# Optimization experiments

Hardware: AMD Instinct MI355X
Metric: run time of the kernel (lower is better)

## Reference

```python
import jax, jax.numpy as jnp
import numpy as np

PAIRS = np.array([[0, 4], [1, 5], [2, 6], [3, 7], [0, 5], [1, 4], [2, 7], [3, 6]])


def setup_inputs() -> dict:
    key = jax.random.key(0)
    ks = jax.random.split(key, 40)
    rn = lambda k, shape: (jax.random.normal(k, shape, jnp.float32) * 0.05)
    inp = {
        "waiting": jax.random.uniform(ks[0], (1, 8), jnp.float32),
        "phase": jax.random.uniform(ks[1], (1, 8), jnp.float32),
        "wtime_mu": jax.random.uniform(ks[2], (1, 8), jnp.float32),
        "wtime_sigma": jax.random.uniform(ks[3], (1, 8), jnp.float32),
        "wtime_max": jax.random.uniform(ks[4], (1, 8), jnp.float32),
        "i_position": jax.random.uniform(ks[5], (1, 1), jnp.float32),
        "j_position": jax.random.uniform(ks[6], (1, 1), jnp.float32),
        # NN_demand: 14 -> 256 -> 32 -> 4
        "d_w1": rn(ks[7], (256, 14)), "d_b1": rn(ks[8], (256,)),
        "d_w2": rn(ks[9], (32, 256)), "d_b2": rn(ks[10], (32,)),
        "d_w3": rn(ks[11], (4, 32)), "d_b3": rn(ks[12], (4,)),
        # NN_coupled_demand: 8 -> 128 -> 32 -> 4
        "c_w1": rn(ks[13], (128, 8)), "c_b1": rn(ks[14], (128,)),
        "c_w2": rn(ks[15], (32, 128)), "c_b2": rn(ks[16], (32,)),
        "c_w3": rn(ks[17], (4, 32)), "c_b3": rn(ks[18], (4,)),
        # Conv_D: 1x1 convs 8 -> 256 -> 32 -> 2
        "dD_w1": rn(ks[19], (256, 8)), "dD_b1": rn(ks[20], (256,)),
        "dD_w2": rn(ks[21], (32, 256)), "dD_b2": rn(ks[22], (32,)),
        "dD_w3": rn(ks[23], (2, 32)), "dD_b3": rn(ks[24], (2,)),
        # Conv_C: 1x1 convs 3 -> 256 -> 32 -> 8, then (1,7) conv 8 -> 1
        "cC_w1": rn(ks[25], (256, 3)), "cC_b1": rn(ks[26], (256,)),
        "cC_w2": rn(ks[27], (32, 256)), "cC_b2": rn(ks[28], (32,)),
        "cC_w3": rn(ks[29], (8, 32)), "cC_b3": rn(ks[30], (8,)),
        "cC_w4": rn(ks[31], (8, 7)), "cC_b4": rn(ks[32], (1,)),
    }
    return inp


def _mlp3(x, w1, b1, w2, b2, w3, b3):
    h = jax.nn.relu(x @ w1.T + b1)
    h = jax.nn.relu(h @ w2.T + b2)
    return h @ w3.T + b3


def _frap_forward(waiting, phase, wtime_mu, wtime_sigma, wtime_max, i_position, j_position,
                  d_w1, d_b1, d_w2, d_b2, d_w3, d_b3,
                  c_w1, c_b1, c_w2, c_b2, c_w3, c_b3,
                  dD_w1, dD_b1, dD_w2, dD_b2, dD_w3, dD_b3,
                  cC_w1, cC_b1, cC_w2, cC_b2, cC_w3, cC_b3, cC_w4, cC_b4):
    pairs = jnp.asarray(PAIRS)
    # per-lane demand features: (8, 14) = [i, j, mu_l, sigma_l, max_l, wait_l, phase(8)]
    feat = jnp.concatenate([
        jnp.broadcast_to(i_position[0], (8, 1)),
        jnp.broadcast_to(j_position[0], (8, 1)),
        wtime_mu[0, :, None], wtime_sigma[0, :, None],
        wtime_max[0, :, None], waiting[0, :, None],
        jnp.broadcast_to(phase[0][None, :], (8, 8)),
    ], axis=1)
    demand = _mlp3(feat, d_w1, d_b1, d_w2, d_b2, d_w3, d_b3)  # (8, 4)
    # coupled demand per phase pair: (8, 8) -> (8, 4)
    vec = jnp.concatenate([demand[pairs[:, 0]], demand[pairs[:, 1]]], axis=1)
    dp = _mlp3(vec, c_w1, c_b1, c_w2, c_b2, c_w3, c_b3)  # (8, 4)
    # D tensor (8, 8, 7): D[0:4, i, k] = dp[i]; D[4:8, i, k] = dp[j(k)], j(k)=k + (k>=i)
    k = jnp.arange(7)
    i = jnp.arange(8)
    j_idx = k[None, :] + (k[None, :] >= i[:, None]).astype(jnp.int32)  # (8, 7)
    top = jnp.broadcast_to(dp.T[:, :, None], (4, 8, 7))
    bot = jnp.transpose(dp[j_idx], (2, 0, 1))  # (4, 8, 7)
    D = jnp.concatenate([top, bot], axis=0)  # (8, 8, 7)
    # Conv_D: 1x1 convs are channel matmuls on (C, H, W)
    h = jax.nn.relu(jnp.einsum('oc,chw->ohw', dD_w1, D) + dD_b1[:, None, None])
    h = jax.nn.relu(jnp.einsum('oc,chw->ohw', dD_w2, h) + dD_b2[:, None, None])
    H_d = jnp.einsum('oc,chw->ohw', dD_w3, h) + dD_b3[:, None, None]  # (2, 8, 7)
    comp = jnp.zeros((1, 8, 7), H_d.dtype)
    H_c = jnp.concatenate([H_d, comp], axis=0)  # (3, 8, 7)
    # Conv_C
    h = jax.nn.relu(jnp.einsum('oc,chw->ohw', cC_w1, H_c) + cC_b1[:, None, None])
    h = jax.nn.relu(jnp.einsum('oc,chw->ohw', cC_w2, h) + cC_b2[:, None, None])
    h = jax.nn.relu(jnp.einsum('oc,chw->ohw', cC_w3, h) + cC_b3[:, None, None])  # (8, 8, 7)
    # conv4: kernel (1,7), out (1, 8, 1); return C[0, :, 0] -> (8,)
    out = jnp.einsum('cw,chw->h', cC_w4, h) + cC_b4[0]
    return out


def reference(waiting, phase, wtime_mu, wtime_sigma, wtime_max, i_position, j_position,
              d_w1, d_b1, d_w2, d_b2, d_w3, d_b3,
              c_w1, c_b1, c_w2, c_b2, c_w3, c_b3,
              dD_w1, dD_b1, dD_w2, dD_b2, dD_w3, dD_b3,
              cC_w1, cC_b1, cC_w2, cC_b2, cC_w3, cC_b3, cC_w4, cC_b4):
    return _frap_forward(waiting, phase, wtime_mu, wtime_sigma, wtime_max, i_position, j_position,
                         d_w1, d_b1, d_w2, d_b2, d_w3, d_b3,
                         c_w1, c_b1, c_w2, c_b2, c_w3, c_b3,
                         dD_w1, dD_b1, dD_w2, dD_b2, dD_w3, dD_b3,
                         cC_w1, cC_b1, cC_w2, cC_b2, cC_w3, cC_b3, cC_w4, cC_b4)
```

## Files before the change

kernel.cpp:

```cpp
#include <hip/hip_runtime.h>


#define DEV __device__ __forceinline__

#define WAVE_SYNC() do { \
    asm volatile("s_waitcnt lgkmcnt(0)" ::: "memory"); \
    __builtin_amdgcn_sched_barrier(0); \
} while (0)

DEV float dot4a(float acc, float4 a, float4 b) {
    acc = fmaf(a.x, b.x, acc);
    acc = fmaf(a.y, b.y, acc);
    acc = fmaf(a.z, b.z, acc);
    acc = fmaf(a.w, b.w, acc);
    return acc;
}

DEV float warm_arr(const float* __restrict__ p, int n4, int id, float sink) {
    const float4* p4 = (const float4*)p;
    for (int i = id; i < n4; i += 448) {
        float4 v = p4[i];
        sink += v.x + v.y + v.z + v.w;
    }
    return sink;
}

DEV void conv_h2_vec(const float* __restrict__ big, const float* __restrict__ w2g,
                     const float* __restrict__ b2g, float* __restrict__ mid, int t)
{
    int kq = t & 1;
    int u  = t >> 1;
    int ch = u >> 3, sl = u & 7;
    float a0 = 0.0f, a1 = 0.0f, a2 = 0.0f, a3 = 0.0f;
    if (sl < 7) {
        const float4* wp = (const float4*)(w2g + ch * 256) + kq * 32;
        const float* hrow = big + (sl << 8);
#pragma unroll 2
        for (int g = 0; g < 32; g += 4) {
            int gg = kq * 32 + g;
            float4 w0 = wp[g + 0], w1 = wp[g + 1], w2 = wp[g + 2], w3 = wp[g + 3];
            float4 h0 = *(const float4*)(hrow + (((gg + 0) ^ sl) << 2));
            float4 h1 = *(const float4*)(hrow + (((gg + 1) ^ sl) << 2));
            float4 h2 = *(const float4*)(hrow + (((gg + 2) ^ sl) << 2));
            float4 h3v = *(const float4*)(hrow + (((gg + 3) ^ sl) << 2));
            a0 = dot4a(a0, h0, w0);
            a1 = dot4a(a1, h1, w1);
            a2 = dot4a(a2, h2, w2);
            a3 = dot4a(a3, h3v, w3);
        }
    }
    float r = (a0 + a1) + (a2 + a3);
    r += __shfl_xor(r, 1);
    if (sl < 7 && kq == 0)
        mid[ch * 7 + sl] = fmaxf(r + b2g[ch], 0.0f);
}

__global__ __launch_bounds__(512, 1) void frap_kernel(
    const float* __restrict__ waiting, const float* __restrict__ phase,
    const float* __restrict__ wtime_mu, const float* __restrict__ wtime_sigma,
    const float* __restrict__ wtime_max,
    const float* __restrict__ i_pos, const float* __restrict__ j_pos,
    const float* __restrict__ d_w1, const float* __restrict__ d_b1,
    const float* __restrict__ d_w2, const float* __restrict__ d_b2,
    const float* __restrict__ d_w3, const float* __restrict__ d_b3,
    const float* __restrict__ c_w1, const float* __restrict__ c_b1,
    const float* __restrict__ c_w2, const float* __restrict__ c_b2,
    const float* __restrict__ c_w3, const float* __restrict__ c_b3,
    const float* __restrict__ dD_w1, const float* __restrict__ dD_b1,
    const float* __restrict__ dD_w2, const float* __restrict__ dD_b2,
    const float* __restrict__ dD_w3, const float* __restrict__ dD_b3,
    const float* __restrict__ cC_w1, const float* __restrict__ cC_b1,
    const float* __restrict__ cC_w2, const float* __restrict__ cC_b2,
    const float* __restrict__ cC_w3, const float* __restrict__ cC_b3,
    const float* __restrict__ cC_w4, const float* __restrict__ cC_b4,
    float* __restrict__ out)
{
    __shared__ __align__(16) float sm[4096];
    const int t  = threadIdx.x;
    const int wg = blockIdx.x;
    const int ln = t & 63;

    float* feat16 = sm;
    float* dh1  = sm + 128;
    float* dh2  = sm + 2176;
    float* dem  = sm + 2432;
    float* ch1  = sm + 2464;
    float* ch2  = sm + 3488;
    float* big  = sm;
    float* mid  = sm + 3744;
    float* dp   = sm + 3968;
    float* Hd   = sm + 4000;
    float* h3   = sm;

    if (t < 64) {
        for (int rep = 0; rep < 2; ++rep) {
            int idx = rep * 64 + ln;
            int l = idx >> 4, c = idx & 15;
            float v = 0.0f;
            if      (c == 0) v = i_pos[0];
            else if (c == 1) v = j_pos[0];
            else if (c == 2) v = wtime_mu[l];
            else if (c == 3) v = wtime_sigma[l];
            else if (c == 4) v = wtime_max[l];
            else if (c == 5) v = waiting[l];
            else if (c < 14) v = phase[c - 6];
            feat16[idx] = v;
        }
        WAVE_SYNC();

        for (int q = 0; q < 4; ++q) {
            int o = q * 64 + ln;
            const float* w = d_w1 + o * 14;
            float w0 = w[0], w1 = w[1], w2 = w[2], w3 = w[3], w4 = w[4];
            float w5 = w[5], w6 = w[6], w7 = w[7], w8 = w[8], w9 = w[9];
            float wa = w[10], wb = w[11], wc = w[12], wd = w[13];
            float bias = d_b1[o];
#pragma unroll
            for (int l = 0; l < 8; ++l) {
                const float4* f4 = (const float4*)(feat16 + l * 16);
                float4 f0 = f4[0], f1 = f4[1], f2 = f4[2], f3 = f4[3];
                float acc = bias;
                acc = fmaf(f0.x, w0, acc); acc = fmaf(f0.y, w1, acc);
                acc = fmaf(f0.z, w2, acc); acc = fmaf(f0.w, w3, acc);
                acc = fmaf(f1.x, w4, acc); acc = fmaf(f1.y, w5, acc);
                acc = fmaf(f1.z, w6, acc); acc = fmaf(f1.w, w7, acc);
                acc = fmaf(f2.x, w8, acc); acc = fmaf(f2.y, w9, acc);
                acc = fmaf(f2.z, wa, acc); acc = fmaf(f2.w, wb, acc);
                acc = fmaf(f3.x, wc, acc); acc = fmaf(f3.y, wd, acc);
                dh1[l * 256 + o] = fmaxf(acc, 0.0f);
            }
        }
        WAVE_SYNC();

        {
            int o = ln & 31, lh = ln >> 5;
            float acc0 = 0.0f, acc1 = 0.0f, acc2 = 0.0f, acc3 = 0.0f;
            const float4* w4p = (const float4*)(d_w2 + o * 256);
#pragma unroll 4
            for (int cb = 0; cb < 64; ++cb) {
                float4 w = w4p[cb];
                float4 h0 = *(const float4*)(dh1 + (lh * 4 + 0) * 256 + cb * 4);
                float4 h1 = *(const float4*)(dh1 + (lh * 4 + 1) * 256 + cb * 4);
                float4 h2 = *(const float4*)(dh1 + (lh * 4 + 2) * 256 + cb * 4);
                float4 h3v = *(const float4*)(dh1 + (lh * 4 + 3) * 256 + cb * 4);
                acc0 = dot4a(acc0, h0, w);
                acc1 = dot4a(acc1, h1, w);
                acc2 = dot4a(acc2, h2, w);
                acc3 = dot4a(acc3, h3v, w);
            }
            float b = d_b2[o];
            dh2[(lh * 4 + 0) * 32 + o] = fmaxf(acc0 + b, 0.0f);
            dh2[(lh * 4 + 1) * 32 + o] = fmaxf(acc1 + b, 0.0f);
            dh2[(lh * 4 + 2) * 32 + o] = fmaxf(acc2 + b, 0.0f);
            dh2[(lh * 4 + 3) * 32 + o] = fmaxf(acc3 + b, 0.0f);
        }
        WAVE_SYNC();

        if (ln < 32) {
            int l = ln >> 2, o = ln & 3;
            const float4* w = (const float4*)(d_w3 + o * 32);
            const float4* h = (const float4*)(dh2 + l * 32);
            float acc = d_b3[o];
#pragma unroll
            for (int g = 0; g < 8; ++g) acc = dot4a(acc, h[g], w[g]);
            dem[ln] = acc;
        }
        WAVE_SYNC();

        for (int rep = 0; rep < 2; ++rep) {
            int o = rep * 64 + ln;
            const float4* w = (const float4*)(c_w1 + o * 8);
            float4 w0 = w[0], w1 = w[1];
            float bias = c_b1[o];
#pragma unroll
            for (int p = 0; p < 8; ++p) {
                int a0 = p & 3;
                int a1 = (p < 4) ? (4 + (p & 3)) : (4 + ((p & 3) ^ 1));
                float4 va = *(const float4*)(dem + a0 * 4);
                float4 vb = *(const float4*)(dem + a1 * 4);
                float acc = dot4a(dot4a(bias, va, w0), vb, w1);
                ch1[p * 128 + o] = fmaxf(acc, 0.0f);
            }
        }
        WAVE_SYNC();

        {
            int o = ln & 31, lh = ln >> 5;
            float acc0 = 0.0f, acc1 = 0.0f, acc2 = 0.0f, acc3 = 0.0f;
            const float4* w4p = (const float4*)(c_w2 + o * 128);
#pragma unroll 4
            for (int cb = 0; cb < 32; ++cb) {
                float4 w = w4p[cb];
                float4 h0 = *(const float4*)(ch1 + (lh * 4 + 0) * 128 + cb * 4);
                float4 h1 = *(const float4*)(ch1 + (lh * 4 + 1) * 128 + cb * 4);
                float4 h2 = *(const float4*)(ch1 + (lh * 4 + 2) * 128 + cb * 4);
                float4 h3v = *(const float4*)(ch1 + (lh * 4 + 3) * 128 + cb * 4);
                acc0 = dot4a(acc0, h0, w);
                acc1 = dot4a(acc1, h1, w);
                acc2 = dot4a(acc2, h2, w);
                acc3 = dot4a(acc3, h3v, w);
            }
            float b = c_b2[o];
            ch2[(lh * 4 + 0) * 32 + o] = fmaxf(acc0 + b, 0.0f);
            ch2[(lh * 4 + 1) * 32 + o] = fmaxf(acc1 + b, 0.0f);
            ch2[(lh * 4 + 2) * 32 + o] = fmaxf(acc2 + b, 0.0f);
            ch2[(lh * 4 + 3) * 32 + o] = fmaxf(acc3 + b, 0.0f);
        }
        WAVE_SYNC();

        if (ln < 32) {
            int l = ln >> 2, o = ln & 3;
            const float4* w = (const float4*)(c_w3 + o * 32);
            const float4* h = (const float4*)(ch2 + l * 32);
            float acc = c_b3[o];
#pragma unroll
            for (int g = 0; g < 8; ++g) acc = dot4a(acc, h[g], w[g]);
            dp[ln] = acc;
        }
    } else {
        int id = t - 64;
        float snk = 0.0f;
        snk = warm_arr(d_w1,  896, id, snk);
        snk = warm_arr(d_b1,   64, id, snk);
        snk = warm_arr(d_w2, 2048, id, snk);
        snk = warm_arr(d_b2,    8, id, snk);
        snk = warm_arr(d_w3,   32, id, snk);
        snk = warm_arr(d_b3,    1, id, snk);
        snk = warm_arr(c_w1,  256, id, snk);
        snk = warm_arr(c_b1,   32, id, snk);
        snk = warm_arr(c_w2, 1024, id, snk);
        snk = warm_arr(c_b2,    8, id, snk);
        snk = warm_arr(c_w3,   32, id, snk);
        snk = warm_arr(c_b3,    1, id, snk);
        snk = warm_arr(dD_w1, 512, id, snk);
        snk = warm_arr(dD_b1,  64, id, snk);
        snk = warm_arr(dD_w2, 2048, id, snk);
        snk = warm_arr(dD_b2,   8, id, snk);
        snk = warm_arr(dD_w3,  16, id, snk);
        snk = warm_arr(cC_w1, 192, id, snk);
        snk = warm_arr(cC_b1,  64, id, snk);
        snk = warm_arr(cC_w2, 2048, id, snk);
        snk = warm_arr(cC_b2,   8, id, snk);
        snk = warm_arr(cC_w3,  64, id, snk);
        snk = warm_arr(cC_b3,   2, id, snk);
        snk = warm_arr(cC_w4,  14, id, snk);
        asm volatile("" :: "v"(snk));
    }
    __syncthreads();

    {
        const float4* dp4 = (const float4*)dp;
        int o = t & 255;
        const float4* wrow = (const float4*)(dD_w1 + o * 8);
        float4 w0 = wrow[0], w1 = wrow[1];
        float bias = dD_b1[o];
        float4 di = dp4[wg];
#pragma unroll
        for (int it = 0; it < 4; ++it) {
            int sl = (t >> 8) + it * 2;
            if (sl < 7) {
                int j = sl + (sl >= wg ? 1 : 0);
                float acc = dot4a(dot4a(bias, di, w0), dp4[j], w1);
                big[(sl << 8) + (((o >> 2) ^ sl) << 2) + (o & 3)] = fmaxf(acc, 0.0f);
            }
        }
    }
    __syncthreads();

    conv_h2_vec(big, dD_w2, dD_b2, mid, t);
    __syncthreads();

    if (t < 56) {
        int kq = t & 3, u = t >> 2;
        int o = (u >= 7) ? 1 : 0;
        int s = u - o * 7;
        float acc = 0.0f;
#pragma unroll
        for (int cc = 0; cc < 8; ++cc) {
            int c = kq * 8 + cc;
            acc = fmaf(mid[c * 7 + s], dD_w3[o * 32 + c], acc);
        }
        acc += __shfl_xor(acc, 1);
        acc += __shfl_xor(acc, 2);
        if (kq == 0) Hd[o * 7 + s] = acc + dD_b3[o];
    }
    __syncthreads();

    {
        int o = t & 255;
        float w0 = cC_w1[o * 3], w1 = cC_w1[o * 3 + 1];
        float bias = cC_b1[o];
#pragma unroll
        for (int it = 0; it < 4; ++it) {
            int sl = (t >> 8) + it * 2;
            if (sl < 7) {
                float acc = fmaf(Hd[7 + sl], w1, fmaf(Hd[sl], w0, bias));
                big[(sl << 8) + (((o >> 2) ^ sl) << 2) + (o & 3)] = fmaxf(acc, 0.0f);
            }
        }
    }
    __syncthreads();

    conv_h2_vec(big, cC_w2, cC_b2, mid, t);
    __syncthreads();

    if (t < 224) {
        int kq = t & 3, u = t >> 2;
        int o = u & 7, s = u >> 3;
        float acc = 0.0f;
#pragma unroll
        for (int cc = 0; cc < 8; ++cc) {
            int c = kq * 8 + cc;
            acc = fmaf(mid[c * 7 + s], cC_w3[o * 32 + c], acc);
        }
        acc += __shfl_xor(acc, 1);
        acc += __shfl_xor(acc, 2);
        if (kq == 0) h3[o * 7 + s] = fmaxf(acc + cC_b3[o], 0.0f);
    }
    __syncthreads();

    if (t < 64) {
        float p = 0.0f;
        if (ln < 56) {
            int c = ln / 7, w = ln % 7;
            p = cC_w4[c * 7 + w] * h3[c * 7 + w];
        }
#pragma unroll
        for (int off = 1; off < 64; off <<= 1) p += __shfl_xor(p, off);
        if (ln == 0) out[wg] = p + cC_b4[0];
    }
}

extern "C" void kernel_launch(void* const* d_in, const int* in_sizes, int n_in,
                              void* d_out, int out_size, void* d_ws, size_t ws_size,
                              hipStream_t stream) {
    (void)in_sizes; (void)n_in; (void)d_ws; (void)ws_size; (void)out_size;
    const float* a[33];
    for (int i = 0; i < 33; ++i) a[i] = (const float*)d_in[i];
    frap_kernel<<<dim3(8), dim3(512), 0, stream>>>(
        a[0], a[1], a[2], a[3], a[4], a[5], a[6],
        a[7], a[8], a[9], a[10], a[11], a[12],
        a[13], a[14], a[15], a[16], a[17], a[18],
        a[19], a[20], a[21], a[22], a[23], a[24],
        a[25], a[26], a[27], a[28], a[29], a[30], a[31], a[32],
        (float*)d_out);
}
```

Baseline: 26.35 us.

## Assign one wave per spatial column to run the conv chain without block barriers

Restructures the Conv_D/Conv_C stages so each of 7 waves handles one spatial position end to end, chaining the layers with wave-local LDS waits instead of several block-wide __syncthreads. Each wave's partial of the final (1,7) conv goes to shared memory, and a single thread sums the seven partials. This removes about six block barriers and the cross-position shared layout. In exchange, each wave now does serial work (64 lanes per 256-wide layer), leaves one of the eight waves idle, and makes each wave reload the weights itself.

```diff
diff --git a/kernel.cpp b/kernel.cpp
--- a/kernel.cpp
+++ b/kernel.cpp
@@ -23,36 +23,6 @@
         sink += v.x + v.y + v.z + v.w;
     }
     return sink;
-}
-
-DEV void conv_h2_vec(const float* __restrict__ big, const float* __restrict__ w2g,
-                     const float* __restrict__ b2g, float* __restrict__ mid, int t)
-{
-    int kq = t & 1;
-    int u  = t >> 1;
-    int ch = u >> 3, sl = u & 7;
-    float a0 = 0.0f, a1 = 0.0f, a2 = 0.0f, a3 = 0.0f;
-    if (sl < 7) {
-        const float4* wp = (const float4*)(w2g + ch * 256) + kq * 32;
-        const float* hrow = big + (sl << 8);
-#pragma unroll 2
-        for (int g = 0; g < 32; g += 4) {
-            int gg = kq * 32 + g;
-            float4 w0 = wp[g + 0], w1 = wp[g + 1], w2 = wp[g + 2], w3 = wp[g + 3];
-            float4 h0 = *(const float4*)(hrow + (((gg + 0) ^ sl) << 2));
-            float4 h1 = *(const float4*)(hrow + (((gg + 1) ^ sl) << 2));
-            float4 h2 = *(const float4*)(hrow + (((gg + 2) ^ sl) << 2));
-            float4 h3v = *(const float4*)(hrow + (((gg + 3) ^ sl) << 2));
-            a0 = dot4a(a0, h0, w0);
-            a1 = dot4a(a1, h1, w1);
-            a2 = dot4a(a2, h2, w2);
-            a3 = dot4a(a3, h3v, w3);
-        }
-    }
-    float r = (a0 + a1) + (a2 + a3);
-    r += __shfl_xor(r, 1);
-    if (sl < 7 && kq == 0)
-        mid[ch * 7 + sl] = fmaxf(r + b2g[ch], 0.0f);
 }
 
 __global__ __launch_bounds__(512, 1) void frap_kernel(
@@ -86,11 +56,12 @@
     float* dem  = sm + 2432;
     float* ch1  = sm + 2464;
     float* ch2  = sm + 3488;
-    float* big  = sm;
-    float* mid  = sm + 3744;
+    float* conv_h1   = sm;
+    float* conv_mid  = sm + 1792;
+    float* conv_mid2 = sm + 2016;
+    float* conv_Hd   = sm + 2240;
+    float* partial   = sm + 2254;
     float* dp   = sm + 3968;
-    float* Hd   = sm + 4000;
-    float* h3   = sm;
 
     if (t < 64) {
         for (int rep = 0; rep < 2; ++rep) {
@@ -249,85 +220,105 @@
     __syncthreads();
 
     {
-        const float4* dp4 = (const float4*)dp;
-        int o = t & 255;
-        const float4* wrow = (const float4*)(dD_w1 + o * 8);
-        float4 w0 = wrow[0], w1 = wrow[1];
-        float bias = dD_b1[o];
-        float4 di = dp4[wg];
-#pragma unroll
-        for (int it = 0; it < 4; ++it) {
-            int sl = (t >> 8) + it * 2;
-            if (sl < 7) {
-                int j = sl + (sl >= wg ? 1 : 0);
-                float acc = dot4a(dot4a(bias, di, w0), dp4[j], w1);
-                big[(sl << 8) + (((o >> 2) ^ sl) << 2) + (o & 3)] = fmaxf(acc, 0.0f);
+        int w = t >> 6;
+        if (w < 7) {
+            const int j = w + (w >= wg ? 1 : 0);
+            float* h1row = conv_h1  + w * 256;
+            float* midp  = conv_mid + w * 32;
+            float* mid2p = conv_mid2 + w * 32;
+            float* Hdp   = conv_Hd  + w * 2;
+
+            const float4* dp4 = (const float4*)dp;
+            float4 di = dp4[wg], dj = dp4[j];
+#pragma unroll
+            for (int q = 0; q < 4; ++q) {
+                int o = q * 64 + ln;
+                const float4* wrow = (const float4*)(dD_w1 + o * 8);
+                float acc = dot4a(dot4a(dD_b1[o], di, wrow[0]), dj, wrow[1]);
+                h1row[o] = fmaxf(acc, 0.0f);
+            }
+            WAVE_SYNC();
+
+            {
+                int ch = ln >> 1, kq = ln & 1;
+                const float4* wp = (const float4*)(dD_w2 + ch * 256) + kq * 32;
+                const float4* hp = (const float4*)h1row + kq * 32;
+                float a0 = 0.0f, a1 = 0.0f, a2 = 0.0f, a3 = 0.0f;
+#pragma unroll 2
+                for (int e = 0; e < 32; e += 4) {
+                    a0 = dot4a(a0, hp[e + 0], wp[e + 0]);
+                    a1 = dot4a(a1, hp[e + 1], wp[e + 1]);
+                    a2 = dot4a(a2, hp[e + 2], wp[e + 2]);
+                    a3 = dot4a(a3, hp[e + 3], wp[e + 3]);
+                }
+                float r = (a0 + a1) + (a2 + a3);
+                r += __shfl_xor(r, 1);
+                if (kq == 0) midp[ch] = fmaxf(r + dD_b2[ch], 0.0f);
+            }
+            WAVE_SYNC();
+
+            if (ln < 2) {
+                const float4* wp = (const float4*)(dD_w3 + ln * 32);
+                const float4* mp = (const float4*)midp;
+                float acc = dD_b3[ln];
+#pragma unroll
+                for (int g = 0; g < 8; ++g) acc = dot4a(acc, mp[g], wp[g]);
+                Hdp[ln] = acc;
+            }
+            WAVE_SYNC();
+
+            {
+                float h0 = Hdp[0], h1v = Hdp[1];
+#pragma unroll
+                for (int q = 0; q < 4; ++q) {
+                    int o = q * 64 + ln;
+                    float acc = fmaf(h1v, cC_w1[o * 3 + 1],
+                                     fmaf(h0, cC_w1[o * 3], cC_b1[o]));
+                    h1row[o] = fmaxf(acc, 0.0f);
+                }
+            }
+            WAVE_SYNC();
+
+            {
+                int ch = ln >> 1, kq = ln & 1;
+                const float4* wp = (const float4*)(cC_w2 + ch * 256) + kq * 32;
+                const float4* hp = (const float4*)h1row + kq * 32;
+                float a0 = 0.0f, a1 = 0.0f, a2 = 0.0f, a3 = 0.0f;
+#pragma unroll 2
+                for (int e = 0; e < 32; e += 4) {
+                    a0 = dot4a(a0, hp[e + 0], wp[e + 0]);
+                    a1 = dot4a(a1, hp[e + 1], wp[e + 1]);
+                    a2 = dot4a(a2, hp[e + 2], wp[e + 2]);
+                    a3 = dot4a(a3, hp[e + 3], wp[e + 3]);
+                }
+                float r = (a0 + a1) + (a2 + a3);
+                r += __shfl_xor(r, 1);
+                if (kq == 0) mid2p[ch] = fmaxf(r + cC_b2[ch], 0.0f);
+            }
+            WAVE_SYNC();
+
+            if (ln < 8) {
+                const float4* wp = (const float4*)(cC_w3 + ln * 32);
+                const float4* mp = (const float4*)mid2p;
+                float acc = cC_b3[ln];
+#pragma unroll
+                for (int g = 0; g < 8; ++g) acc = dot4a(acc, mp[g], wp[g]);
+                float h3v = fmaxf(acc, 0.0f);
+                float p = cC_w4[ln * 7 + w] * h3v;
+                p += __shfl_xor(p, 1);
+                p += __shfl_xor(p, 2);
+                p += __shfl_xor(p, 4);
+                if (ln == 0) partial[w] = p;
             }
         }
     }
     __syncthreads();
 
-    conv_h2_vec(big, dD_w2, dD_b2, mid, t);
-    __syncthreads();
-
-    if (t < 56) {
-        int kq = t & 3, u = t >> 2;
-        int o = (u >= 7) ? 1 : 0;
-        int s = u - o * 7;
-        float acc = 0.0f;
-#pragma unroll
-        for (int cc = 0; cc < 8; ++cc) {
-            int c = kq * 8 + cc;
-            acc = fmaf(mid[c * 7 + s], dD_w3[o * 32 + c], acc);
-        }
-        acc += __shfl_xor(acc, 1);
-        acc += __shfl_xor(acc, 2);
-        if (kq == 0) Hd[o * 7 + s] = acc + dD_b3[o];
-    }
-    __syncthreads();
-
-    {
-        int o = t & 255;
-        float w0 = cC_w1[o * 3], w1 = cC_w1[o * 3 + 1];
-        float bias = cC_b1[o];
-#pragma unroll
-        for (int it = 0; it < 4; ++it) {
-            int sl = (t >> 8) + it * 2;
-            if (sl < 7) {
-                float acc = fmaf(Hd[7 + sl], w1, fmaf(Hd[sl], w0, bias));
-                big[(sl << 8) + (((o >> 2) ^ sl) << 2) + (o & 3)] = fmaxf(acc, 0.0f);
-            }
-        }
-    }
-    __syncthreads();
-
-    conv_h2_vec(big, cC_w2, cC_b2, mid, t);
-    __syncthreads();
-
-    if (t < 224) {
-        int kq = t & 3, u = t >> 2;
-        int o = u & 7, s = u >> 3;
-        float acc = 0.0f;
-#pragma unroll
-        for (int cc = 0; cc < 8; ++cc) {
-            int c = kq * 8 + cc;
-            acc = fmaf(mid[c * 7 + s], cC_w3[o * 32 + c], acc);
-        }
-        acc += __shfl_xor(acc, 1);
-        acc += __shfl_xor(acc, 2);
-        if (kq == 0) h3[o * 7 + s] = fmaxf(acc + cC_b3[o], 0.0f);
-    }
-    __syncthreads();
-
-    if (t < 64) {
-        float p = 0.0f;
-        if (ln < 56) {
-            int c = ln / 7, w = ln % 7;
-            p = cC_w4[c * 7 + w] * h3[c * 7 + w];
-        }
-#pragma unroll
-        for (int off = 1; off < 64; off <<= 1) p += __shfl_xor(p, off);
-        if (ln == 0) out[wg] = p + cC_b4[0];
+    if (t == 0) {
+        float s = cC_b4[0];
+#pragma unroll
+        for (int w = 0; w < 7; ++w) s += partial[w];
+        out[wg] = s;
     }
 }
 
```

Result: slower. 30.98 us (+17.6%).

## Split demand MLPs across two waves and fuse Conv_D tail into Conv_C input

Applied to the files above, without the earlier changes.

The demand and coupled-demand MLP stages now run on two waves, each handling half the rows, with a block barrier between the two MLPs. Cache warming moves to the remaining waves and is split across those phases. The Conv_D final layer is fused with the Conv_C first layer per wave, which removes one block barrier. The Conv_C final layer is likewise fused with the (1,7) conv through per-wave partial sums, removing another barrier. The trade-off is an extra __syncthreads between the MLPs and redundant per-wave recomputation of Hd.

```diff
diff --git a/kernel.cpp b/kernel.cpp
--- a/kernel.cpp
+++ b/kernel.cpp
@@ -18,7 +18,7 @@
 
 DEV float warm_arr(const float* __restrict__ p, int n4, int id, float sink) {
     const float4* p4 = (const float4*)p;
-    for (int i = id; i < n4; i += 448) {
+    for (int i = id; i < n4; i += 384) {
         float4 v = p4[i];
         sink += v.x + v.y + v.z + v.w;
     }
@@ -78,6 +78,7 @@
     __shared__ __align__(16) float sm[4096];
     const int t  = threadIdx.x;
     const int wg = blockIdx.x;
+    const int wv = t >> 6;
     const int ln = t & 63;
 
     float* feat16 = sm;
@@ -86,15 +87,15 @@
     float* dem  = sm + 2432;
     float* ch1  = sm + 2464;
     float* ch2  = sm + 3488;
-    float* big  = sm;
-    float* mid  = sm + 3744;
     float* dp   = sm + 3968;
-    float* Hd   = sm + 4000;
-    float* h3   = sm;
-
-    if (t < 64) {
-        for (int rep = 0; rep < 2; ++rep) {
-            int idx = rep * 64 + ln;
+    float* convh   = sm;
+    float* mid     = sm + 1792;
+    float* partial = sm + 2016;
+
+    if (wv < 2) {
+        const int wbase = wv * 4;
+        {
+            int idx = wv * 64 + ln;
             int l = idx >> 4, c = idx & 15;
             float v = 0.0f;
             if      (c == 0) v = i_pos[0];
@@ -116,7 +117,8 @@
             float wa = w[10], wb = w[11], wc = w[12], wd = w[13];
             float bias = d_b1[o];
 #pragma unroll
-            for (int l = 0; l < 8; ++l) {
+            for (int r = 0; r < 4; ++r) {
+                int l = wbase + r;
                 const float4* f4 = (const float4*)(feat16 + l * 16);
                 float4 f0 = f4[0], f1 = f4[1], f2 = f4[2], f3 = f4[3];
                 float acc = bias;
@@ -134,91 +136,34 @@
 
         {
             int o = ln & 31, lh = ln >> 5;
-            float acc0 = 0.0f, acc1 = 0.0f, acc2 = 0.0f, acc3 = 0.0f;
+            int r0 = wbase + lh * 2, r1 = r0 + 1;
+            float acc0 = 0.0f, acc1 = 0.0f;
             const float4* w4p = (const float4*)(d_w2 + o * 256);
 #pragma unroll 4
             for (int cb = 0; cb < 64; ++cb) {
                 float4 w = w4p[cb];
-                float4 h0 = *(const float4*)(dh1 + (lh * 4 + 0) * 256 + cb * 4);
-                float4 h1 = *(const float4*)(dh1 + (lh * 4 + 1) * 256 + cb * 4);
-                float4 h2 = *(const float4*)(dh1 + (lh * 4 + 2) * 256 + cb * 4);
-                float4 h3v = *(const float4*)(dh1 + (lh * 4 + 3) * 256 + cb * 4);
+                float4 h0 = *(const float4*)(dh1 + r0 * 256 + cb * 4);
+                float4 h1 = *(const float4*)(dh1 + r1 * 256 + cb * 4);
                 acc0 = dot4a(acc0, h0, w);
                 acc1 = dot4a(acc1, h1, w);
-                acc2 = dot4a(acc2, h2, w);
-                acc3 = dot4a(acc3, h3v, w);
             }
             float b = d_b2[o];
-            dh2[(lh * 4 + 0) * 32 + o] = fmaxf(acc0 + b, 0.0f);
-            dh2[(lh * 4 + 1) * 32 + o] = fmaxf(acc1 + b, 0.0f);
-            dh2[(lh * 4 + 2) * 32 + o] = fmaxf(acc2 + b, 0.0f);
-            dh2[(lh * 4 + 3) * 32 + o] = fmaxf(acc3 + b, 0.0f);
-        }
-        WAVE_SYNC();
-
-        if (ln < 32) {
-            int l = ln >> 2, o = ln & 3;
+            dh2[r0 * 32 + o] = fmaxf(acc0 + b, 0.0f);
+            dh2[r1 * 32 + o] = fmaxf(acc1 + b, 0.0f);
+        }
+        WAVE_SYNC();
+
+        if (ln < 16) {
+            int l = wbase + (ln >> 2), o = ln & 3;
             const float4* w = (const float4*)(d_w3 + o * 32);
             const float4* h = (const float4*)(dh2 + l * 32);
             float acc = d_b3[o];
 #pragma unroll
             for (int g = 0; g < 8; ++g) acc = dot4a(acc, h[g], w[g]);
-            dem[ln] = acc;
-        }
-        WAVE_SYNC();
-
-        for (int rep = 0; rep < 2; ++rep) {
-            int o = rep * 64 + ln;
-            const float4* w = (const float4*)(c_w1 + o * 8);
-            float4 w0 = w[0], w1 = w[1];
-            float bias = c_b1[o];
-#pragma unroll
-            for (int p = 0; p < 8; ++p) {
-                int a0 = p & 3;
-                int a1 = (p < 4) ? (4 + (p & 3)) : (4 + ((p & 3) ^ 1));
-                float4 va = *(const float4*)(dem + a0 * 4);
-                float4 vb = *(const float4*)(dem + a1 * 4);
-                float acc = dot4a(dot4a(bias, va, w0), vb, w1);
-                ch1[p * 128 + o] = fmaxf(acc, 0.0f);
-            }
-        }
-        WAVE_SYNC();
-
-        {
-            int o = ln & 31, lh = ln >> 5;
-            float acc0 = 0.0f, acc1 = 0.0f, acc2 = 0.0f, acc3 = 0.0f;
-            const float4* w4p = (const float4*)(c_w2 + o * 128);
-#pragma unroll 4
-            for (int cb = 0; cb < 32; ++cb) {
-                float4 w = w4p[cb];
-                float4 h0 = *(const float4*)(ch1 + (lh * 4 + 0) * 128 + cb * 4);
-                float4 h1 = *(const float4*)(ch1 + (lh * 4 + 1) * 128 + cb * 4);
-                float4 h2 = *(const float4*)(ch1 + (lh * 4 + 2) * 128 + cb * 4);
-                float4 h3v = *(const float4*)(ch1 + (lh * 4 + 3) * 128 + cb * 4);
-                acc0 = dot4a(acc0, h0, w);
-                acc1 = dot4a(acc1, h1, w);
-                acc2 = dot4a(acc2, h2, w);
-                acc3 = dot4a(acc3, h3v, w);
-            }
-            float b = c_b2[o];
-            ch2[(lh * 4 + 0) * 32 + o] = fmaxf(acc0 + b, 0.0f);
-            ch2[(lh * 4 + 1) * 32 + o] = fmaxf(acc1 + b, 0.0f);
-            ch2[(lh * 4 + 2) * 32 + o] = fmaxf(acc2 + b, 0.0f);
-            ch2[(lh * 4 + 3) * 32 + o] = fmaxf(acc3 + b, 0.0f);
-        }
-        WAVE_SYNC();
-
-        if (ln < 32) {
-            int l = ln >> 2, o = ln & 3;
-            const float4* w = (const float4*)(c_w3 + o * 32);
-            const float4* h = (const float4*)(ch2 + l * 32);
-            float acc = c_b3[o];
-#pragma unroll
-            for (int g = 0; g < 8; ++g) acc = dot4a(acc, h[g], w[g]);
-            dp[ln] = acc;
+            dem[l * 4 + o] = acc;
         }
     } else {
-        int id = t - 64;
+        int id = t - 128;
         float snk = 0.0f;
         snk = warm_arr(d_w1,  896, id, snk);
         snk = warm_arr(d_b1,   64, id, snk);
@@ -232,18 +177,73 @@
         snk = warm_arr(c_b2,    8, id, snk);
         snk = warm_arr(c_w3,   32, id, snk);
         snk = warm_arr(c_b3,    1, id, snk);
-        snk = warm_arr(dD_w1, 512, id, snk);
-        snk = warm_arr(dD_b1,  64, id, snk);
+        asm volatile("" :: "v"(snk));
+    }
+    __syncthreads();
+
+    if (wv < 2) {
+        const int pbase = wv * 4;
+        for (int rep = 0; rep < 2; ++rep) {
+            int o = rep * 64 + ln;
+            const float4* w = (const float4*)(c_w1 + o * 8);
+            float4 w0 = w[0], w1 = w[1];
+            float bias = c_b1[o];
+#pragma unroll
+            for (int pp = 0; pp < 4; ++pp) {
+                int p = pbase + pp;
+                int a0 = p & 3;
+                int a1 = (p < 4) ? (4 + (p & 3)) : (4 + ((p & 3) ^ 1));
+                float4 va = *(const float4*)(dem + a0 * 4);
+                float4 vb = *(const float4*)(dem + a1 * 4);
+                float acc = dot4a(dot4a(bias, va, w0), vb, w1);
+                ch1[p * 128 + o] = fmaxf(acc, 0.0f);
+            }
+        }
+        WAVE_SYNC();
+
+        {
+            int o = ln & 31, lh = ln >> 5;
+            int r0 = pbase + lh * 2, r1 = r0 + 1;
+            float acc0 = 0.0f, acc1 = 0.0f;
+            const float4* w4p = (const float4*)(c_w2 + o * 128);
+#pragma unroll 4
+            for (int cb = 0; cb < 32; ++cb) {
+                float4 w = w4p[cb];
+                float4 h0 = *(const float4*)(ch1 + r0 * 128 + cb * 4);
+                float4 h1 = *(const float4*)(ch1 + r1 * 128 + cb * 4);
+                acc0 = dot4a(acc0, h0, w);
+                acc1 = dot4a(acc1, h1, w);
+            }
+            float b = c_b2[o];
+            ch2[r0 * 32 + o] = fmaxf(acc0 + b, 0.0f);
+            ch2[r1 * 32 + o] = fmaxf(acc1 + b, 0.0f);
+        }
+        WAVE_SYNC();
+
+        if (ln < 16) {
+            int p = pbase + (ln >> 2), o = ln & 3;
+            const float4* w = (const float4*)(c_w3 + o * 32);
+            const float4* h = (const float4*)(ch2 + p * 32);
+            float acc = c_b3[o];
+#pragma unroll
+            for (int g = 0; g < 8; ++g) acc = dot4a(acc, h[g], w[g]);
+            dp[p * 4 + o] = acc;
+        }
+    } else {
+        int id = t - 128;
+        float snk = 0.0f;
+        snk = warm_arr(dD_w1,  512, id, snk);
+        snk = warm_arr(dD_b1,   64, id, snk);
         snk = warm_arr(dD_w2, 2048, id, snk);
-        snk = warm_arr(dD_b2,   8, id, snk);
-        snk = warm_arr(dD_w3,  16, id, snk);
-        snk = warm_arr(cC_w1, 192, id, snk);
-        snk = warm_arr(cC_b1,  64, id, snk);
+        snk = warm_arr(dD_b2,    8, id, snk);
+        snk = warm_arr(dD_w3,   16, id, snk);
+        snk = warm_arr(cC_w1,  192, id, snk);
+        snk = warm_arr(cC_b1,   64, id, snk);
         snk = warm_arr(cC_w2, 2048, id, snk);
-        snk = warm_arr(cC_b2,   8, id, snk);
-        snk = warm_arr(cC_w3,  64, id, snk);
-        snk = warm_arr(cC_b3,   2, id, snk);
-        snk = warm_arr(cC_w4,  14, id, snk);
+        snk = warm_arr(cC_b2,    8, id, snk);
+        snk = warm_arr(cC_w3,   64, id, snk);
+        snk = warm_arr(cC_b3,    2, id, snk);
+        snk = warm_arr(cC_w4,   14, id, snk);
         asm volatile("" :: "v"(snk));
     }
     __syncthreads();
@@ -261,73 +261,74 @@
             if (sl < 7) {
                 int j = sl + (sl >= wg ? 1 : 0);
                 float acc = dot4a(dot4a(bias, di, w0), dp4[j], w1);
-                big[(sl << 8) + (((o >> 2) ^ sl) << 2) + (o & 3)] = fmaxf(acc, 0.0f);
-            }
-        }
-    }
-    __syncthreads();
-
-    conv_h2_vec(big, dD_w2, dD_b2, mid, t);
-    __syncthreads();
-
-    if (t < 56) {
-        int kq = t & 3, u = t >> 2;
-        int o = (u >= 7) ? 1 : 0;
-        int s = u - o * 7;
-        float acc = 0.0f;
+                convh[(sl << 8) + (((o >> 2) ^ sl) << 2) + (o & 3)] = fmaxf(acc, 0.0f);
+            }
+        }
+    }
+    __syncthreads();
+
+    conv_h2_vec(convh, dD_w2, dD_b2, mid, t);
+    __syncthreads();
+
+    if (wv < 7) {
+        const int w = wv;
+        float s00 = 0.0f, s01 = 0.0f, s02 = 0.0f, s03 = 0.0f;
+        float s10 = 0.0f, s11 = 0.0f, s12 = 0.0f, s13 = 0.0f;
 #pragma unroll
         for (int cc = 0; cc < 8; ++cc) {
-            int c = kq * 8 + cc;
-            acc = fmaf(mid[c * 7 + s], dD_w3[o * 32 + c], acc);
-        }
-        acc += __shfl_xor(acc, 1);
-        acc += __shfl_xor(acc, 2);
-        if (kq == 0) Hd[o * 7 + s] = acc + dD_b3[o];
-    }
-    __syncthreads();
-
-    {
-        int o = t & 255;
-        float w0 = cC_w1[o * 3], w1 = cC_w1[o * 3 + 1];
-        float bias = cC_b1[o];
-#pragma unroll
-        for (int it = 0; it < 4; ++it) {
-            int sl = (t >> 8) + it * 2;
-            if (sl < 7) {
-                float acc = fmaf(Hd[7 + sl], w1, fmaf(Hd[sl], w0, bias));
-                big[(sl << 8) + (((o >> 2) ^ sl) << 2) + (o & 3)] = fmaxf(acc, 0.0f);
-            }
-        }
-    }
-    __syncthreads();
-
-    conv_h2_vec(big, cC_w2, cC_b2, mid, t);
-    __syncthreads();
-
-    if (t < 224) {
-        int kq = t & 3, u = t >> 2;
-        int o = u & 7, s = u >> 3;
-        float acc = 0.0f;
+            float m0 = mid[(0 * 8 + cc) * 7 + w];
+            float m1 = mid[(1 * 8 + cc) * 7 + w];
+            float m2 = mid[(2 * 8 + cc) * 7 + w];
+            float m3 = mid[(3 * 8 + cc) * 7 + w];
+            s00 = fmaf(m0, dD_w3[0 * 32 + 0 * 8 + cc], s00);
+            s01 = fmaf(m1, dD_w3[0 * 32 + 1 * 8 + cc], s01);
+            s02 = fmaf(m2, dD_w3[0 * 32 + 2 * 8 + cc], s02);
+            s03 = fmaf(m3, dD_w3[0 * 32 + 3 * 8 + cc], s03);
+            s10 = fmaf(m0, dD_w3[1 * 32 + 0 * 8 + cc], s10);
+            s11 = fmaf(m1, dD_w3[1 * 32 + 1 * 8 + cc], s11);
+            s12 = fmaf(m2, dD_w3[1 * 32 + 2 * 8 + cc], s12);
+            s13 = fmaf(m3, dD_w3[1 * 32 + 3 * 8 + cc], s13);
+        }
+        float hd0 = ((s00 + s01) + (s02 + s03)) + dD_b3[0];
+        float hd1 = ((s10 + s11) + (s12 + s13)) + dD_b3[1];
+#pragma unroll
+        for (int q = 0; q < 4; ++q) {
+            int o = q * 64 + ln;
+            float acc = fmaf(hd1, cC_w1[o * 3 + 1],
+                             fmaf(hd0, cC_w1[o * 3], cC_b1[o]));
+            convh[(w << 8) + (((o >> 2) ^ w) << 2) + (o & 3)] = fmaxf(acc, 0.0f);
+        }
+    }
+    __syncthreads();
+
+    conv_h2_vec(convh, cC_w2, cC_b2, mid, t);
+    __syncthreads();
+
+    if (wv < 7 && ln < 8) {
+        const int w = wv;
+        const int o = ln;
+        float s0 = 0.0f, s1 = 0.0f, s2 = 0.0f, s3 = 0.0f;
 #pragma unroll
         for (int cc = 0; cc < 8; ++cc) {
-            int c = kq * 8 + cc;
-            acc = fmaf(mid[c * 7 + s], cC_w3[o * 32 + c], acc);
-        }
-        acc += __shfl_xor(acc, 1);
-        acc += __shfl_xor(acc, 2);
-        if (kq == 0) h3[o * 7 + s] = fmaxf(acc + cC_b3[o], 0.0f);
-    }
-    __syncthreads();
-
-    if (t < 64) {
-        float p = 0.0f;
-        if (ln < 56) {
-            int c = ln / 7, w = ln % 7;
-            p = cC_w4[c * 7 + w] * h3[c * 7 + w];
-        }
-#pragma unroll
-        for (int off = 1; off < 64; off <<= 1) p += __shfl_xor(p, off);
-        if (ln == 0) out[wg] = p + cC_b4[0];
+            s0 = fmaf(mid[(0 * 8 + cc) * 7 + w], cC_w3[o * 32 + 0 * 8 + cc], s0);
+            s1 = fmaf(mid[(1 * 8 + cc) * 7 + w], cC_w3[o * 32 + 1 * 8 + cc], s1);
+            s2 = fmaf(mid[(2 * 8 + cc) * 7 + w], cC_w3[o * 32 + 2 * 8 + cc], s2);
+            s3 = fmaf(mid[(3 * 8 + cc) * 7 + w], cC_w3[o * 32 + 3 * 8 + cc], s3);
+        }
+        float h3v = fmaxf(((s0 + s1) + (s2 + s3)) + cC_b3[o], 0.0f);
+        float p = cC_w4[o * 7 + w] * h3v;
+        p += __shfl_xor(p, 1);
+        p += __shfl_xor(p, 2);
+        p += __shfl_xor(p, 4);
+        if (o == 0) partial[w] = p;
+    }
+    __syncthreads();
+
+    if (t == 0) {
+        float s = cC_b4[0];
+#pragma unroll
+        for (int w = 0; w < 7; ++w) s += partial[w];
+        out[wg] = s;
     }
 }
 
```

Measured after the change: 25.88 us, median of 2. No clear change (-1.8%).
